# Optimization experiments

Measured on AMD Instinct MI355X. Metric: run time of the kernel, lower is better.

Reference implementation:

```python
import jax, jax.numpy as jnp
import numpy as np

ALPHA = 1.0

def setup_inputs() -> dict:
    key = jax.random.key(0)
    k1, k2 = jax.random.split(key)
    N, D, K = 262144, 64, 256
    x = jax.random.normal(k1, (N, D), dtype=jnp.float32)
    clusters = jax.random.normal(k2, (K, D), dtype=jnp.float32)
    return {"x": x, "clusters": clusters}

def reference(x, clusters):
    # Pairwise squared distances via GEMM decomposition:
    x_sq = jnp.sum(x * x, axis=1, keepdims=True)            # (N, 1)
    c_sq = jnp.sum(clusters * clusters, axis=1)             # (K,)
    cross = x @ clusters.T                                  # (N, K)
    sq_dist = x_sq - 2.0 * cross + c_sq[None, :]            # (N, K)
    # Student-t kernel
    q = 1.0 / (1.0 + sq_dist / ALPHA)
    q = q ** ((ALPHA + 1.0) / 2.0)
    # Row normalize
    q = q / jnp.sum(q, axis=1, keepdims=True)
    return q
```

## Files before the change

kernel.cpp:

```cpp
#include <hip/hip_runtime.h>

#define NKC 256
#define ND  64

using v8bf = __attribute__((ext_vector_type(8))) __bf16;
using v4f  = __attribute__((ext_vector_type(4))) float;
using v4u  = __attribute__((ext_vector_type(4))) unsigned int;

__device__ __forceinline__ unsigned short f2bf(float f) {
    unsigned int x = __float_as_uint(f);
    x += 0x7FFFu + ((x >> 16) & 1u);
    return (unsigned short)(x >> 16);
}

__global__ void prep_kernel(const float* __restrict__ clusters,
                            unsigned short* __restrict__ cbf,
                            float* __restrict__ csq) {
    int t = threadIdx.x;
    int lane = t & 63;
    int row = blockIdx.x * 4 + (t >> 6);
    float v = clusters[row * ND + lane];
    cbf[row * ND + lane] = f2bf(v);
    float p = v * v;
#pragma unroll
    for (int m = 1; m <= 32; m <<= 1) p += __shfl_xor(p, m);
    if (lane == 0) csq[row] = p;
}

__global__ __launch_bounds__(256, 4)
void cluster_kernel(const float* __restrict__ x,
                    const unsigned short* __restrict__ cbf,
                    const float* __restrict__ csq,
                    float* __restrict__ out) {
    __shared__ __align__(16) unsigned short sc[NKC * ND];
    __shared__ float scsq[NKC];

    const int t = threadIdx.x;

    {
        char* dst = (char*)sc;
        const char* src = (const char*)cbf;
#pragma unroll
        for (int i = 0; i < 8; ++i) {
            int byte = (t + i * 256) << 4;
            int crow = byte >> 7;
            v4u val = *(const v4u*)(src + byte);
            *(v4u*)(dst + (byte ^ ((crow & 7) << 4))) = val;
        }
        scsq[t] = csq[t];
    }
    __syncthreads();

    const int lane = t & 63;
    const int wid  = t >> 6;
    const int lr   = lane & 15;
    const int hi   = lane >> 4;
    const int kg   = hi << 3;

    const int row = blockIdx.x * 64 + wid * 16 + lr;
    const float* xp = x + (size_t)row * ND + kg;
    v4f x00 = *(const v4f*)(xp);
    v4f x01 = *(const v4f*)(xp + 4);
    v4f x10 = *(const v4f*)(xp + 32);
    v4f x11 = *(const v4f*)(xp + 36);

    float v0[8], v1[8];
    *(v4f*)&v0[0] = x00; *(v4f*)&v0[4] = x01;
    *(v4f*)&v1[0] = x10; *(v4f*)&v1[4] = x11;

    float p = 0.f;
#pragma unroll
    for (int i = 0; i < 8; ++i) p += v0[i] * v0[i] + v1[i] * v1[i];
    p += __shfl_xor(p, 16);
    p += __shfl_xor(p, 32);

    v4u u0, u1;
#pragma unroll
    for (int i = 0; i < 4; ++i) {
        u0[i] = (unsigned)f2bf(v0[2 * i]) | ((unsigned)f2bf(v0[2 * i + 1]) << 16);
        u1[i] = (unsigned)f2bf(v1[2 * i]) | ((unsigned)f2bf(v1[2 * i + 1]) << 16);
    }
    v8bf a0 = *(v8bf*)&u0;
    v8bf a1 = *(v8bf*)&u1;

    v4f acc[16];
#pragma unroll
    for (int j = 0; j < 16; ++j) {
        const int brow = (j << 4) + lr;
        const int bswz = (brow & 7) << 4;
        v8bf c0 = *(v8bf*)((char*)sc + ((brow * 128      + kg * 2) ^ bswz));
        v8bf c1 = *(v8bf*)((char*)sc + ((brow * 128 + 64 + kg * 2) ^ bswz));
        v4f c = {0.f, 0.f, 0.f, 0.f};
        c = __builtin_amdgcn_mfma_f32_16x16x32_bf16(c0, a0, c, 0, 0, 0);
        c = __builtin_amdgcn_mfma_f32_16x16x32_bf16(c1, a1, c, 0, 0, 0);
        acc[j] = c;
    }

    float ps = 0.f;
#pragma unroll
    for (int j = 0; j < 16; ++j) {
        v4f cs = *(const v4f*)&scsq[(j << 4) + (hi << 2)];
#pragma unroll
        for (int r = 0; r < 4; ++r) {
            float d = p + cs[r] - 2.0f * acc[j][r];
            float u = __builtin_amdgcn_rcpf(1.0f + d);
            acc[j][r] = u;
            ps += u;
        }
    }
    ps += __shfl_xor(ps, 16);
    ps += __shfl_xor(ps, 32);
    const float inv = __builtin_amdgcn_rcpf(ps);
#pragma unroll
    for (int j = 0; j < 16; ++j) {
#pragma unroll
        for (int r = 0; r < 4; ++r) acc[j][r] *= inv;
    }

    __syncthreads();

    char* slice = (char*)sc + wid * 8192;
    const int q = lr & 7;
    const int rowbase = blockIdx.x * 64 + wid * 16;
#pragma unroll
    for (int rnd = 0; rnd < 2; ++rnd) {
        if ((lr >> 3) == rnd) {
#pragma unroll
            for (int j = 0; j < 16; ++j) {
                *(v4u*)(slice + q * 1024 + (((j << 6) + (hi << 4)) ^ (q << 4))) =
                    *(v4u*)&acc[j];
            }
        }
        __asm__ volatile("s_waitcnt lgkmcnt(0)" ::: "memory");
#pragma unroll
        for (int q2 = 0; q2 < 8; ++q2) {
            v4u val = *(v4u*)(slice + q2 * 1024 + ((lane << 4) ^ (q2 << 4)));
            float* orow = out + (size_t)(rowbase + rnd * 8 + q2) * NKC;
            *(v4u*)(orow + (lane << 2)) = val;
        }
        __asm__ volatile("s_waitcnt lgkmcnt(0)" ::: "memory");
    }
}

extern "C" void kernel_launch(void* const* d_in, const int* in_sizes, int n_in,
                              void* d_out, int out_size, void* d_ws, size_t ws_size,
                              hipStream_t stream) {
    const float* x        = (const float*)d_in[0];
    const float* clusters = (const float*)d_in[1];
    float* out = (float*)d_out;
    const int N = in_sizes[0] / ND;

    unsigned short* cbf = (unsigned short*)d_ws;
    float* csq = (float*)((char*)d_ws + (size_t)NKC * ND * sizeof(unsigned short));

    prep_kernel<<<NKC / 4, 256, 0, stream>>>(clusters, cbf, csq);
    cluster_kernel<<<N / 64, 256, 0, stream>>>(x, cbf, csq, out);
}
```

Before: 72.22 us.

## Fuse cluster prep into main kernel and use nontemporal output stores

Result: faster. 62.01 us (-14.1%).

```diff
diff --git a/kernel.cpp b/kernel.cpp
--- a/kernel.cpp
+++ b/kernel.cpp
@@ -13,44 +13,14 @@
     return (unsigned short)(x >> 16);
 }
 
-__global__ void prep_kernel(const float* __restrict__ clusters,
-                            unsigned short* __restrict__ cbf,
-                            float* __restrict__ csq) {
-    int t = threadIdx.x;
-    int lane = t & 63;
-    int row = blockIdx.x * 4 + (t >> 6);
-    float v = clusters[row * ND + lane];
-    cbf[row * ND + lane] = f2bf(v);
-    float p = v * v;
-#pragma unroll
-    for (int m = 1; m <= 32; m <<= 1) p += __shfl_xor(p, m);
-    if (lane == 0) csq[row] = p;
-}
-
 __global__ __launch_bounds__(256, 4)
 void cluster_kernel(const float* __restrict__ x,
-                    const unsigned short* __restrict__ cbf,
-                    const float* __restrict__ csq,
+                    const float* __restrict__ clusters,
                     float* __restrict__ out) {
     __shared__ __align__(16) unsigned short sc[NKC * ND];
     __shared__ float scsq[NKC];
 
-    const int t = threadIdx.x;
-
-    {
-        char* dst = (char*)sc;
-        const char* src = (const char*)cbf;
-#pragma unroll
-        for (int i = 0; i < 8; ++i) {
-            int byte = (t + i * 256) << 4;
-            int crow = byte >> 7;
-            v4u val = *(const v4u*)(src + byte);
-            *(v4u*)(dst + (byte ^ ((crow & 7) << 4))) = val;
-        }
-        scsq[t] = csq[t];
-    }
-    __syncthreads();
-
+    const int t    = threadIdx.x;
     const int lane = t & 63;
     const int wid  = t >> 6;
     const int lr   = lane & 15;
@@ -63,6 +33,40 @@
     v4f x01 = *(const v4f*)(xp + 4);
     v4f x10 = *(const v4f*)(xp + 32);
     v4f x11 = *(const v4f*)(xp + 36);
+
+    {
+        const int seg  = t & 3;
+        const int rloc = t >> 2;
+#pragma unroll
+        for (int it = 0; it < 4; ++it) {
+            const int crow = it * 64 + rloc;
+            const float* cp = clusters + crow * ND + seg * 16;
+            v4f c0 = *(const v4f*)(cp);
+            v4f c1 = *(const v4f*)(cp + 4);
+            v4f c2 = *(const v4f*)(cp + 8);
+            v4f c3 = *(const v4f*)(cp + 12);
+            float cv[16];
+            *(v4f*)&cv[0] = c0; *(v4f*)&cv[4] = c1;
+            *(v4f*)&cv[8] = c2; *(v4f*)&cv[12] = c3;
+            float ss = 0.f;
+#pragma unroll
+            for (int i = 0; i < 16; ++i) ss += cv[i] * cv[i];
+            ss += __shfl_xor(ss, 1);
+            ss += __shfl_xor(ss, 2);
+            if (seg == 0) scsq[crow] = ss;
+            v4u w0, w1;
+#pragma unroll
+            for (int i = 0; i < 4; ++i) {
+                w0[i] = (unsigned)f2bf(cv[2*i])   | ((unsigned)f2bf(cv[2*i+1]) << 16);
+                w1[i] = (unsigned)f2bf(cv[8+2*i]) | ((unsigned)f2bf(cv[9+2*i]) << 16);
+            }
+            const int swz = (crow & 7) << 4;
+            const int byte0 = crow * 128 + seg * 32;
+            *(v4u*)((char*)sc + ( byte0       ^ swz)) = w0;
+            *(v4u*)((char*)sc + ((byte0 + 16) ^ swz)) = w1;
+        }
+    }
+    __syncthreads();
 
     float v0[8], v1[8];
     *(v4f*)&v0[0] = x00; *(v4f*)&v0[4] = x01;
@@ -136,7 +140,7 @@
         for (int q2 = 0; q2 < 8; ++q2) {
             v4u val = *(v4u*)(slice + q2 * 1024 + ((lane << 4) ^ (q2 << 4)));
             float* orow = out + (size_t)(rowbase + rnd * 8 + q2) * NKC;
-            *(v4u*)(orow + (lane << 2)) = val;
+            __builtin_nontemporal_store(val, (v4u*)(orow + (lane << 2)));
         }
         __asm__ volatile("s_waitcnt lgkmcnt(0)" ::: "memory");
     }
@@ -150,9 +154,5 @@
     float* out = (float*)d_out;
     const int N = in_sizes[0] / ND;
 
-    unsigned short* cbf = (unsigned short*)d_ws;
-    float* csq = (float*)((char*)d_ws + (size_t)NKC * ND * sizeof(unsigned short));
-
-    prep_kernel<<<NKC / 4, 256, 0, stream>>>(clusters, cbf, csq);
-    cluster_kernel<<<N / 64, 256, 0, stream>>>(x, cbf, csq, out);
+    cluster_kernel<<<N / 64, 256, 0, stream>>>(x, clusters, out);
 }
```
